# Optimization experiments

Measured on AMD Instinct MI355X. Metric: run time of the kernel, lower is better.

Reference implementation:

```python
import jax, jax.numpy as jnp
from jax import lax
import numpy as np

B, L, H, V = 256, 2048, 128, 32000
THR = 0.4      # energy_threshold
LN_EPS = 1e-5  # torch LayerNorm default


def setup_inputs() -> dict:
    key = jax.random.key(0)
    ks = jax.random.split(key, 12)
    s = lambda k, shp, scale: (jax.random.normal(k, shp, dtype=jnp.float32) * scale)
    return {
        "seq": jax.random.randint(ks[0], (B, L), 0, V),
        "embed": s(ks[1], (V, H), 0.02),
        "W1": s(ks[2], (H, 2 * H), H ** -0.5),
        "b1": jnp.zeros((2 * H,), jnp.float32),
        "W2": s(ks[3], (2 * H, H), (2 * H) ** -0.5),
        "b2": jnp.zeros((H,), jnp.float32),
        "gamma": jnp.ones((H,), jnp.float32),
        "beta": jnp.zeros((H,), jnp.float32),
        "Wrp": s(ks[4], (H, H), H ** -0.5),
        "brp": jnp.zeros((H,), jnp.float32),
        "Wout": s(ks[5], (H, V), H ** -0.5),
        "bout": jnp.zeros((V,), jnp.float32),
    }


def _encode(seq, embed, W1, b1, W2, b2, gamma, beta):
    e = embed[seq]                                         # [B,L,H]
    ff = jnp.maximum(e @ W1 + b1, 0.0) @ W2 + b2           # [B,L,H]
    y = e + ff
    mu = y.mean(-1, keepdims=True)
    var = ((y - mu) ** 2).mean(-1, keepdims=True)
    return (y - mu) * lax.rsqrt(var + LN_EPS) * gamma + beta


def reference(seq, embed, W1, b1, W2, b2, gamma, beta, Wrp, brp, Wout, bout):
    h_all = _encode(seq, embed, W1, b1, W2, b2, gamma, beta)  # [B,L,H]

    def step(M, k):
        # k = v = h_all[:, t, :]  -> [B,H]
        v = k
        vp = jnp.einsum('bij,bj->bi', M, k)
        error = v - vp / (jnp.sum(k * k, axis=-1, keepdims=True) + 1e-6)
        gate = (jnp.linalg.norm(error, axis=-1)
                > THR * jnp.linalg.norm(v, axis=-1)).astype(M.dtype)  # [B]
        M = M + gate[:, None, None] * jnp.einsum('bi,bj->bij', error, k)
        return M, None

    M0 = jnp.zeros((B, H, H), h_all.dtype)
    ks = jnp.swapaxes(h_all[:, :-1, :], 0, 1)               # [L-1,B,H]
    M_fin, _ = lax.scan(step, M0, ks)
    r = jnp.einsum('bij,bj->bi', M_fin, h_all[:, -1, :])    # [B,H]
    return (r @ Wrp + brp) @ Wout + bout                    # [B,V]
```

## Files before the change

kernel.cpp:

```cpp
#include <hip/hip_runtime.h>
#include <hip/hip_bf16.h>


#define BB 256
#define LL 2048
#define HH 128
#define VV 32000
#define RS 136

typedef float f32x2 __attribute__((ext_vector_type(2)));

__device__ __forceinline__ void dma16(const float* g, float* l) {
  __builtin_amdgcn_global_load_lds(
      (const __attribute__((address_space(1))) void*)g,
      (__attribute__((address_space(3))) void*)l,
      16, 0, 0);
}

template <int CTRL>
__device__ __forceinline__ float dppadd(float x) {
  int y = __builtin_amdgcn_update_dpp(0, __float_as_int(x), CTRL, 0xF, 0xF, true);
  return x + __int_as_float(y);
}

__device__ __forceinline__ void pkfma(f32x2& d, f32x2 a, f32x2 b) {
  asm("v_pk_fma_f32 %0, %1, %2, %0" : "+v"(d) : "v"(a), "v"(b));
}

__device__ __forceinline__ void barrier_lgkm() {
  asm volatile("s_waitcnt lgkmcnt(0)\n\ts_barrier" ::: "memory");
}
__device__ __forceinline__ void wait_vm1() {
  asm volatile("s_waitcnt vmcnt(1)" ::: "memory");
}
__device__ __forceinline__ void wait_vm0() {
  asm volatile("s_waitcnt vmcnt(0)" ::: "memory");
}

__global__ __launch_bounds__(256, 1) void build_htab_kernel(
    const float* __restrict__ embed,
    const float* __restrict__ W1,
    const float* __restrict__ b1,
    const float* __restrict__ W2,
    const float* __restrict__ b2,
    const float* __restrict__ gamma,
    const float* __restrict__ beta,
    float* __restrict__ Htab2)
{
  const int tid = threadIdx.x;
  const int j   = tid & 127;
  const int h2  = tid >> 7;

  float w1r[128];
#pragma unroll
  for (int m = 0; m < 128; ++m) w1r[m] = W1[m * 256 + tid];

  const float b1n = b1[tid];
  const float b2j = b2[j];
  const float gj  = gamma[j];
  const float bj  = beta[j];

  __shared__ __align__(16) float4 w2q[64][128];
  __shared__ __align__(16) float e_s[128];
  __shared__ __align__(16) float a_s[256];
  __shared__ float p_s[2][128];
  __shared__ float red[8];

  for (int idx = tid; idx < 8192; idx += 256) {
    int n4 = idx >> 7, jj = idx & 127;
    float4 w;
    w.x = W2[(size_t)(4 * n4 + 0) * 128 + jj];
    w.y = W2[(size_t)(4 * n4 + 1) * 128 + jj];
    w.z = W2[(size_t)(4 * n4 + 2) * 128 + jj];
    w.w = W2[(size_t)(4 * n4 + 3) * 128 + jj];
    w2q[n4][jj] = w;
  }
  __syncthreads();

  for (int v = blockIdx.x; v < VV; v += gridDim.x) {
    if (tid < 128) e_s[tid] = embed[(size_t)v * 128 + tid];
    __syncthreads();

    float acc[4] = {b1n, 0.f, 0.f, 0.f};
#pragma unroll
    for (int q = 0; q < 32; ++q) {
      float4 ev = *(const float4*)&e_s[4 * q];
      float t = ev.x * w1r[4 * q + 0];
      t = fmaf(ev.y, w1r[4 * q + 1], t);
      t = fmaf(ev.z, w1r[4 * q + 2], t);
      t = fmaf(ev.w, w1r[4 * q + 3], t);
      acc[q & 3] += t;
    }
    float a = fmaxf((acc[0] + acc[1]) + (acc[2] + acc[3]), 0.0f);
    a_s[tid] = a;
    __syncthreads();

    float p0 = 0.f, p1 = 0.f, p2v = 0.f, p3 = 0.f;
#pragma unroll
    for (int q = 0; q < 32; ++q) {
      int n4 = h2 * 32 + q;
      float4 av = *(const float4*)&a_s[4 * n4];
      float4 wq = w2q[n4][j];
      p0 = fmaf(av.x, wq.x, p0);
      p1 = fmaf(av.y, wq.y, p1);
      p2v = fmaf(av.z, wq.z, p2v);
      p3 = fmaf(av.w, wq.w, p3);
    }
    p_s[h2][j] = (p0 + p1) + (p2v + p3);
    __syncthreads();

    float y = 0.0f;
    if (tid < 128) {
      float ff = p_s[0][tid] + p_s[1][tid] + b2j;
      y = e_s[tid] + ff;
    }
    float s1 = y, s2 = y * y;
    s1 = dppadd<0xB1>(s1);  s2 = dppadd<0xB1>(s2);
    s1 = dppadd<0x4E>(s1);  s2 = dppadd<0x4E>(s2);
    s1 = dppadd<0x141>(s1); s2 = dppadd<0x141>(s2);
    s1 = dppadd<0x140>(s1); s2 = dppadd<0x140>(s2);
    s1 = dppadd<0x142>(s1); s2 = dppadd<0x142>(s2);
    s1 = dppadd<0x143>(s1); s2 = dppadd<0x143>(s2);
    if (tid < 128 && (tid & 63) == 63) {
      red[tid >> 6] = s1;
      red[2 + (tid >> 6)] = s2;
    }
    __syncthreads();
    float mu = (red[0] + red[1]) * (1.0f / 128.0f);
    float ms = (red[2] + red[3]) * (1.0f / 128.0f);
    float var = ms - mu * mu;
    float hv = 0.0f;
    if (tid < 128) {
      float dy = y - mu;
      hv = dy * (1.0f / sqrtf(var + 1e-5f)) * gj + bj;
      int ofs = tid + ((tid >> 6) << 2);
      Htab2[(size_t)v * RS + ofs] = hv;
    }
    float q2 = hv * hv;
    q2 = dppadd<0xB1>(q2);
    q2 = dppadd<0x4E>(q2);
    q2 = dppadd<0x141>(q2);
    q2 = dppadd<0x140>(q2);
    q2 = dppadd<0x142>(q2);
    q2 = dppadd<0x143>(q2);
    if (tid < 128 && (tid & 63) == 63) red[4 + (tid >> 6)] = q2;
    __syncthreads();
    if (tid == 0) {
      float kk = red[4] + red[5];
      Htab2[(size_t)v * RS + 132] = kk;
      Htab2[(size_t)v * RS + 133] = 1.0f / (kk + 1e-6f);
    }
    __syncthreads();
  }
}

__global__ __launch_bounds__(256, 1) void scan_kernel(
    const int* __restrict__ seq,
    const float* __restrict__ Htab2,
    const float* __restrict__ Wrp,
    const float* __restrict__ brp,
    float* __restrict__ rr)
{
  const int b     = blockIdx.x;
  const int tid   = threadIdx.x;
  const int i     = tid >> 1;
  const int half  = tid & 1;
  const int lane  = tid & 63;
  const int wv    = tid >> 6;
  const int iofs  = i + ((i >> 6) << 2);
  const int kbase = half * 68;

  __shared__ int seq_s[LL];
  __shared__ __align__(16) float slots[3][RS];
  __shared__ __align__(16) float red_s[3][4];
  __shared__ __align__(16) float r_s[128];
  __shared__ float p2_s[2][128];

  {
    int t0 = seq[(size_t)b * LL + 0];
    int t1 = seq[(size_t)b * LL + 1];
    if (lane < 34) {
      dma16(Htab2 + (size_t)t0 * RS + lane * 4, &slots[0][0]);
      dma16(Htab2 + (size_t)t1 * RS + lane * 4, &slots[1][0]);
    }
  }
  for (int t = tid; t < LL; t += 256) seq_s[t] = seq[(size_t)b * LL + t];
  __syncthreads();

  f32x2 M2[32];
#pragma unroll
  for (int m = 0; m < 32; ++m) M2[m] = f32x2{0.f, 0.f};

  f32x2 kA[32], kB[32];
  float kiA, kkA, invA, kiB, kkB, invB;
  {
    const float4* kp = (const float4*)&slots[0][kbase];
#pragma unroll
    for (int m = 0; m < 16; ++m) {
      float4 tq = kp[m];
      kA[2 * m]     = f32x2{tq.x, tq.y};
      kA[2 * m + 1] = f32x2{tq.z, tq.w};
    }
    kiA = slots[0][iofs];
    float2 kv = *(const float2*)&slots[0][132];
    kkA = kv.x; invA = kv.y;
#pragma unroll
    for (int m = 0; m < 32; ++m) asm volatile("" : "+v"(kA[m]));
    asm volatile("" : "+v"(kiA), "+v"(kkA), "+v"(invA));
  }

  auto step = [&](f32x2 (&kc)[32], float ki_c, float kk_c, float inv_c,
                  f32x2 (&kn)[32], float& ki_n, float& kk_n, float& inv_n,
                  int t, int p, int sn, int sd, int mode) {
    if (mode == 1) {
      int tk = seq_s[t + 2];
      if (lane < 34)
        dma16(Htab2 + (size_t)tk * RS + lane * 4, &slots[sd][0]);
    }
    f32x2 a0{0.f,0.f}, a1{0.f,0.f}, a2{0.f,0.f}, a3{0.f,0.f};
#pragma unroll
    for (int m = 0; m < 8; ++m) {
      pkfma(a0, kc[4 * m + 0], M2[4 * m + 0]);
      pkfma(a1, kc[4 * m + 1], M2[4 * m + 1]);
      pkfma(a2, kc[4 * m + 2], M2[4 * m + 2]);
      pkfma(a3, kc[4 * m + 3], M2[4 * m + 3]);
    }
    float vp = ((a0.x + a0.y) + (a1.x + a1.y)) + ((a2.x + a2.y) + (a3.x + a3.y));
    vp = dppadd<0xB1>(vp);
    float e = fmaf(-vp, inv_c, ki_c);
    float s = e * e;
    s = dppadd<0x4E>(s);
    s = dppadd<0x141>(s);
    s = dppadd<0x140>(s);
    s = dppadd<0x142>(s);
    s = dppadd<0x143>(s);
    if (lane == 63) red_s[p][wv] = s;
    barrier_lgkm();

    float4 rv = *(const float4*)red_s[p];
    if (mode == 1) wait_vm1(); else wait_vm0();
    {
      const float4* kp = (const float4*)&slots[sn][kbase];
#pragma unroll
      for (int m = 0; m < 16; ++m) {
        float4 tq = kp[m];
        kn[2 * m]     = f32x2{tq.x, tq.y};
        kn[2 * m + 1] = f32x2{tq.z, tq.w};
      }
      ki_n = slots[sn][iofs];
      float2 kv = *(const float2*)&slots[sn][132];
      kk_n = kv.x; inv_n = kv.y;
    }
    float ne2 = (rv.x + rv.y) + (rv.z + rv.w);
    float ge = (ne2 > 0.16f * kk_c) ? e : 0.0f;
    f32x2 ev{ge, ge};
#pragma unroll
    for (int m = 0; m < 32; ++m) pkfma(M2[m], ev, kc[m]);
#pragma unroll
    for (int m = 0; m < 32; ++m) asm volatile("" : "+v"(kn[m]));
    asm volatile("" : "+v"(ki_n), "+v"(kk_n), "+v"(inv_n));
  };

  for (int t = 0; t < LL - 2; t += 6) {
    step(kA, kiA, kkA, invA, kB, kiB, kkB, invB, t + 0, 0, 1, 2, 1);
    step(kB, kiB, kkB, invB, kA, kiA, kkA, invA, t + 1, 1, 2, 0, 1);
    step(kA, kiA, kkA, invA, kB, kiB, kkB, invB, t + 2, 2, 0, 1, 1);
    step(kB, kiB, kkB, invB, kA, kiA, kkA, invA, t + 3, 0, 1, 2, 1);
    step(kA, kiA, kkA, invA, kB, kiB, kkB, invB, t + 4, 1, 2, 0, 1);
    step(kB, kiB, kkB, invB, kA, kiA, kkA, invA, t + 5, 2, 0, 1, 1);
  }
  step(kA, kiA, kkA, invA, kB, kiB, kkB, invB, LL - 2, 0, 1, 2, 2);

  {
    f32x2 a0{0.f,0.f}, a1{0.f,0.f}, a2{0.f,0.f}, a3{0.f,0.f};
#pragma unroll
    for (int m = 0; m < 8; ++m) {
      pkfma(a0, kB[4 * m + 0], M2[4 * m + 0]);
      pkfma(a1, kB[4 * m + 1], M2[4 * m + 1]);
      pkfma(a2, kB[4 * m + 2], M2[4 * m + 2]);
      pkfma(a3, kB[4 * m + 3], M2[4 * m + 3]);
    }
    float vp = ((a0.x + a0.y) + (a1.x + a1.y)) + ((a2.x + a2.y) + (a3.x + a3.y));
    vp = dppadd<0xB1>(vp);
    if (half == 0) r_s[i] = vp;
  }
  __syncthreads();

  const int j  = tid & 127;
  const int h2 = tid >> 7;
  float pac[2] = {0.f, 0.f};
#pragma unroll
  for (int m = 0; m < 64; ++m) {
    pac[m & 1] = fmaf(r_s[h2 * 64 + m],
                      Wrp[(size_t)(h2 * 64 + m) * 128 + j], pac[m & 1]);
  }
  p2_s[h2][j] = pac[0] + pac[1];
  __syncthreads();
  if (tid < 128) {
    rr[(size_t)b * 128 + tid] = p2_s[0][tid] + p2_s[1][tid] + brp[tid];
  }
}

__global__ __launch_bounds__(256, 1) void out_kernel(
    const float* __restrict__ rr,
    const float* __restrict__ Wout,
    const float* __restrict__ bout,
    float* __restrict__ out)
{
  const int tid = threadIdx.x;
  const int v = blockIdx.x * 64 + (tid & 63);
  const int bg = tid >> 6;
  const int b0 = blockIdx.y * 64;

  __shared__ float4 rs4[64][32];
  for (int idx = tid; idx < 2048; idx += 256) {
    int bb = idx >> 5, q = idx & 31;
    rs4[bb][q] = ((const float4*)rr)[(size_t)(b0 + bb) * 32 + q];
  }
  __syncthreads();

  float acc[16];
#pragma unroll
  for (int m = 0; m < 16; ++m) acc[m] = 0.0f;

  for (int h4 = 0; h4 < 32; ++h4) {
    float w0 = Wout[(size_t)(4 * h4 + 0) * VV + v];
    float w1 = Wout[(size_t)(4 * h4 + 1) * VV + v];
    float w2 = Wout[(size_t)(4 * h4 + 2) * VV + v];
    float w3 = Wout[(size_t)(4 * h4 + 3) * VV + v];
#pragma unroll
    for (int m = 0; m < 16; ++m) {
      float4 rv = rs4[bg * 16 + m][h4];
      float t = rv.x * w0;
      t = fmaf(rv.y, w1, t);
      t = fmaf(rv.z, w2, t);
      t = fmaf(rv.w, w3, t);
      acc[m] += t;
    }
  }
  float bo = bout[v];
#pragma unroll
  for (int m = 0; m < 16; ++m) {
    out[(size_t)(b0 + bg * 16 + m) * VV + v] = acc[m] + bo;
  }
}

extern "C" void kernel_launch(void* const* d_in, const int* in_sizes, int n_in,
                              void* d_out, int out_size, void* d_ws, size_t ws_size,
                              hipStream_t stream)
{
  const int* seq      = (const int*)d_in[0];
  const float* embed  = (const float*)d_in[1];
  const float* W1     = (const float*)d_in[2];
  const float* b1     = (const float*)d_in[3];
  const float* W2     = (const float*)d_in[4];
  const float* b2     = (const float*)d_in[5];
  const float* gamma  = (const float*)d_in[6];
  const float* beta   = (const float*)d_in[7];
  const float* Wrp    = (const float*)d_in[8];
  const float* brp    = (const float*)d_in[9];
  const float* Wout   = (const float*)d_in[10];
  const float* bout   = (const float*)d_in[11];
  float* out          = (float*)d_out;

  char* ws = (char*)d_ws;
  float* Htab2 = (float*)ws;
  float* rr    = (float*)(ws + 17408000);

  hipLaunchKernelGGL(build_htab_kernel, dim3(256), dim3(256), 0, stream,
                     embed, W1, b1, W2, b2, gamma, beta, Htab2);
  hipLaunchKernelGGL(scan_kernel, dim3(BB), dim3(256), 0, stream,
                     seq, Htab2, Wrp, brp, rr);
  hipLaunchKernelGGL(out_kernel, dim3(VV / 64, 4), dim3(256), 0, stream,
                     rr, Wout, bout, out);
}
```

Before: 1.473 ms.

## Defer rank-1 memory update and precompute next matvec via dot-product correction

Restructures the recurrent scan step so the M·k_next product is computed before the current gated rank-1 update is applied. The next step then corrects it algebraically with e·(k·k_next), where the dot product is reduced alongside the error norm in the same DPP/LDS reduction. This takes the matvec off the critical dependency chain between the gate decision and the next step's projection. The gate is made wave-uniform, so the rank-1 update can be skipped by a branch when it is off. In exchange it adds a second cross-lane reduction per step, reorders floating-point accumulation, and removes the asm register-pinning hints.

```diff
diff --git a/kernel.cpp b/kernel.cpp
--- a/kernel.cpp
+++ b/kernel.cpp
@@ -172,7 +172,7 @@
 
   __shared__ int seq_s[LL];
   __shared__ __align__(16) float slots[3][RS];
-  __shared__ __align__(16) float red_s[3][4];
+  __shared__ __align__(16) float2 red2[3][4];
   __shared__ __align__(16) float r_s[128];
   __shared__ float p2_s[2][128];
 
@@ -192,7 +192,8 @@
   for (int m = 0; m < 32; ++m) M2[m] = f32x2{0.f, 0.f};
 
   f32x2 kA[32], kB[32];
-  float kiA, kkA, invA, kiB, kkB, invB;
+  float kiA, kkA, invA;
+  float kiB = 0.f, kkB = 0.f, invB = 0.f;
   {
     const float4* kp = (const float4*)&slots[0][kbase];
 #pragma unroll
@@ -204,61 +205,73 @@
     kiA = slots[0][iofs];
     float2 kv = *(const float2*)&slots[0][132];
     kkA = kv.x; invA = kv.y;
-#pragma unroll
-    for (int m = 0; m < 32; ++m) asm volatile("" : "+v"(kA[m]));
-    asm volatile("" : "+v"(kiA), "+v"(kkA), "+v"(invA));
-  }
-
-  auto step = [&](f32x2 (&kc)[32], float ki_c, float kk_c, float inv_c,
-                  f32x2 (&kn)[32], float& ki_n, float& kk_n, float& inv_n,
+  }
+#pragma unroll
+  for (int m = 0; m < 32; ++m) kB[m] = f32x2{0.f, 0.f};
+
+  float vpb = 0.f;
+  float e_prev = 0.f;
+  float ce_prev = 0.f;
+  int   g_prev = 0;
+
+  auto step = [&](f32x2 (&kc)[32], float& ki_c, float& kk_c, float& inv_c,
+                  f32x2 (&ko)[32], float& ki_o, float& kk_o, float& inv_o,
                   int t, int p, int sn, int sd, int mode) {
     if (mode == 1) {
       int tk = seq_s[t + 2];
       if (lane < 34)
         dma16(Htab2 + (size_t)tk * RS + lane * 4, &slots[sd][0]);
     }
-    f32x2 a0{0.f,0.f}, a1{0.f,0.f}, a2{0.f,0.f}, a3{0.f,0.f};
-#pragma unroll
-    for (int m = 0; m < 8; ++m) {
-      pkfma(a0, kc[4 * m + 0], M2[4 * m + 0]);
-      pkfma(a1, kc[4 * m + 1], M2[4 * m + 1]);
-      pkfma(a2, kc[4 * m + 2], M2[4 * m + 2]);
-      pkfma(a3, kc[4 * m + 3], M2[4 * m + 3]);
-    }
-    float vp = ((a0.x + a0.y) + (a1.x + a1.y)) + ((a2.x + a2.y) + (a3.x + a3.y));
-    vp = dppadd<0xB1>(vp);
-    float e = fmaf(-vp, inv_c, ki_c);
-    float s = e * e;
-    s = dppadd<0x4E>(s);
-    s = dppadd<0x141>(s);
-    s = dppadd<0x140>(s);
-    s = dppadd<0x142>(s);
-    s = dppadd<0x143>(s);
-    if (lane == 63) red_s[p][wv] = s;
-    barrier_lgkm();
-
-    float4 rv = *(const float4*)red_s[p];
+    if (g_prev) {
+      f32x2 ev{e_prev, e_prev};
+#pragma unroll
+      for (int m = 0; m < 32; ++m) pkfma(M2[m], ev, ko[m]);
+    }
     if (mode == 1) wait_vm1(); else wait_vm0();
+    float ki_n = slots[sn][iofs];
     {
       const float4* kp = (const float4*)&slots[sn][kbase];
 #pragma unroll
       for (int m = 0; m < 16; ++m) {
         float4 tq = kp[m];
-        kn[2 * m]     = f32x2{tq.x, tq.y};
-        kn[2 * m + 1] = f32x2{tq.z, tq.w};
+        ko[2 * m]     = f32x2{tq.x, tq.y};
+        ko[2 * m + 1] = f32x2{tq.z, tq.w};
       }
-      ki_n = slots[sn][iofs];
       float2 kv = *(const float2*)&slots[sn][132];
-      kk_n = kv.x; inv_n = kv.y;
-    }
-    float ne2 = (rv.x + rv.y) + (rv.z + rv.w);
-    float ge = (ne2 > 0.16f * kk_c) ? e : 0.0f;
-    f32x2 ev{ge, ge};
-#pragma unroll
-    for (int m = 0; m < 32; ++m) pkfma(M2[m], ev, kc[m]);
-#pragma unroll
-    for (int m = 0; m < 32; ++m) asm volatile("" : "+v"(kn[m]));
-    asm volatile("" : "+v"(ki_n), "+v"(kk_n), "+v"(inv_n));
+      kk_o = kv.x; inv_o = kv.y;
+    }
+    float vp = fmaf(ce_prev, e_prev, vpb);
+    float e  = fmaf(-vp, inv_c, ki_c);
+    float s  = e * e;
+    float c1 = ki_c * ki_n;
+    s = dppadd<0x4E>(s);   c1 = dppadd<0x4E>(c1);
+    s = dppadd<0x141>(s);  c1 = dppadd<0x141>(c1);
+    s = dppadd<0x140>(s);  c1 = dppadd<0x140>(c1);
+    s = dppadd<0x142>(s);  c1 = dppadd<0x142>(c1);
+    s = dppadd<0x143>(s);  c1 = dppadd<0x143>(c1);
+    if (lane == 63) red2[p][wv] = float2{s, c1};
+    barrier_lgkm();
+    float4 ra = ((const float4*)&red2[p][0])[0];
+    float4 rb = ((const float4*)&red2[p][0])[1];
+    f32x2 a0{0.f,0.f}, a1{0.f,0.f}, a2{0.f,0.f}, a3{0.f,0.f};
+#pragma unroll
+    for (int m = 0; m < 8; ++m) {
+      pkfma(a0, ko[4 * m + 0], M2[4 * m + 0]);
+      pkfma(a1, ko[4 * m + 1], M2[4 * m + 1]);
+      pkfma(a2, ko[4 * m + 2], M2[4 * m + 2]);
+      pkfma(a3, ko[4 * m + 3], M2[4 * m + 3]);
+    }
+    float nv = ((a0.x + a0.y) + (a1.x + a1.y)) + ((a2.x + a2.y) + (a3.x + a3.y));
+    nv = dppadd<0xB1>(nv);
+    float ne2 = (ra.x + ra.z) + (rb.x + rb.z);
+    float cc  = (ra.y + ra.w) + (rb.y + rb.w);
+    int g = ne2 > 0.16f * kk_c;
+    g = __builtin_amdgcn_readfirstlane(g);
+    g_prev  = g;
+    e_prev  = e;
+    ce_prev = g ? cc : 0.0f;
+    vpb     = nv;
+    ki_o    = ki_n;
   };
 
   for (int t = 0; t < LL - 2; t += 6) {
@@ -272,17 +285,8 @@
   step(kA, kiA, kkA, invA, kB, kiB, kkB, invB, LL - 2, 0, 1, 2, 2);
 
   {
-    f32x2 a0{0.f,0.f}, a1{0.f,0.f}, a2{0.f,0.f}, a3{0.f,0.f};
-#pragma unroll
-    for (int m = 0; m < 8; ++m) {
-      pkfma(a0, kB[4 * m + 0], M2[4 * m + 0]);
-      pkfma(a1, kB[4 * m + 1], M2[4 * m + 1]);
-      pkfma(a2, kB[4 * m + 2], M2[4 * m + 2]);
-      pkfma(a3, kB[4 * m + 3], M2[4 * m + 3]);
-    }
-    float vp = ((a0.x + a0.y) + (a1.x + a1.y)) + ((a2.x + a2.y) + (a3.x + a3.y));
-    vp = dppadd<0xB1>(vp);
-    if (half == 0) r_s[i] = vp;
+    float rres = fmaf(ce_prev, e_prev, vpb);
+    if (half == 0) r_s[i] = rres;
   }
   __syncthreads();
 
```

After: 1.613 ms. 1.09x slower.
